# Optimization experiments

Hardware: AMD Instinct MI355X
Metric: run time of the kernel (lower is better)

The kernel has to match this reference:

```python
import jax, jax.numpy as jnp
import numpy as np

HIDDEN = 4096
NUM_HEADS = 32
NUM_KV_HEADS = 8
HEAD_DIM = 128
ROPE_THETA = 1000000.0
EPS = 1e-6


def setup_inputs() -> dict:
    key = jax.random.key(0)
    ks = jax.random.split(key, 6)
    B, S = 1, 2048
    s = 0.02
    return {
        "hidden_states": jax.random.normal(ks[0], (B, S, HIDDEN), dtype=jnp.float32),
        "position_ids": jnp.arange(B * S, dtype=jnp.int64).reshape(B, S),
        "Wq": jax.random.normal(ks[1], (HIDDEN, NUM_HEADS * HEAD_DIM), dtype=jnp.float32) * s,
        "Wk": jax.random.normal(ks[2], (HIDDEN, NUM_KV_HEADS * HEAD_DIM), dtype=jnp.float32) * s,
        "Wv": jax.random.normal(ks[3], (HIDDEN, NUM_KV_HEADS * HEAD_DIM), dtype=jnp.float32) * s,
        "Wo": jax.random.normal(ks[4], (NUM_HEADS * HEAD_DIM, HIDDEN), dtype=jnp.float32) * s,
        "q_norm_w": jnp.ones((HEAD_DIM,), dtype=jnp.float32),
        "k_norm_w": jnp.ones((HEAD_DIM,), dtype=jnp.float32),
    }


def _rmsnorm(x, w):
    var = jnp.mean(jnp.square(x.astype(jnp.float32)), axis=-1, keepdims=True)
    xn = x * jax.lax.rsqrt(var + EPS)
    return (w * xn).astype(x.dtype)


def _apply_rope(x, positions):
    # x: [b, h, s, d]; positions: [b, s]
    d = x.shape[-1]
    inv_freq = 1.0 / (ROPE_THETA ** (jnp.arange(0, d, 2, dtype=jnp.float32) / d))
    freqs = positions.astype(jnp.float32)[..., None] * inv_freq  # [b, s, d/2]
    cos = jnp.cos(freqs)[:, None].astype(x.dtype)  # [b, 1, s, d/2]
    sin = jnp.sin(freqs)[:, None].astype(x.dtype)
    x1, x2 = x[..., : d // 2], x[..., d // 2 :]
    return jnp.concatenate([x1 * cos - x2 * sin, x2 * cos + x1 * sin], axis=-1)


def reference(hidden_states, position_ids, Wq, Wk, Wv, Wo, q_norm_w, k_norm_w):
    B, S, _ = hidden_states.shape
    groups = NUM_HEADS // NUM_KV_HEADS

    q = (hidden_states @ Wq).reshape(B, S, NUM_HEADS, HEAD_DIM).transpose(0, 2, 1, 3)
    k = (hidden_states @ Wk).reshape(B, S, NUM_KV_HEADS, HEAD_DIM).transpose(0, 2, 1, 3)
    v = (hidden_states @ Wv).reshape(B, S, NUM_KV_HEADS, HEAD_DIM).transpose(0, 2, 1, 3)

    q = _rmsnorm(q, q_norm_w)
    k = _rmsnorm(k, k_norm_w)
    q = _apply_rope(q, position_ids)
    k = _apply_rope(k, position_ids)

    new_k, new_v = k, v  # returned cache (no past_key_value)

    # GQA expansion: [b, kvh, s, d] -> [b, h, s, d]
    kx = jnp.repeat(k, groups, axis=1)
    vx = jnp.repeat(v, groups, axis=1)

    scale = 1.0 / (HEAD_DIM ** 0.5)
    scores = jnp.einsum("bhqd,bhkd->bhqk", q, kx) * scale  # [b, h, s, s]

    kv_len = kx.shape[2]
    row = jnp.arange(S)[:, None]
    col = jnp.arange(kv_len)[None, :]
    causal = col <= row + (kv_len - S)
    scores = jnp.where(causal, scores, -jnp.inf)

    probs = jax.nn.softmax(scores.astype(jnp.float32), axis=-1).astype(q.dtype)
    attn = jnp.einsum("bhqk,bhkd->bhqd", probs, vx)  # [b, h, s, d]
    attn = attn.transpose(0, 2, 1, 3).reshape(B, S, NUM_HEADS * HEAD_DIM)
    out = attn @ Wo
    return out, new_k, new_v, probs
```

## Files before the change

### kernel.cpp

```cpp
#include <hip/hip_runtime.h>
#include <hip/hip_bf16.h>
#include <stdint.h>

#define S_LEN 2048
#define HID   4096
#define NH    32
#define NKV   8
#define HD    128
#define SCALE 0.08838834764831845f

using bf16   = __hip_bfloat16;
using bf16x8 = __attribute__((ext_vector_type(8))) __bf16;
using f32x4  = __attribute__((ext_vector_type(4))) float;

__device__ __forceinline__ void gl2lds(const void* g, void* l) {
  __builtin_amdgcn_global_load_lds(
      (const __attribute__((address_space(1))) unsigned int*)(uintptr_t)g,
      (__attribute__((address_space(3))) unsigned int*)(uintptr_t)l, 16, 0, 0);
}

__device__ __forceinline__ f32x4 mfma16(bf16x8 a, bf16x8 b, f32x4 c) {
  return __builtin_amdgcn_mfma_f32_16x16x32_bf16(a, b, c, 0, 0, 0);
}

__global__ void cast_f32_bf16(const float* __restrict__ in, bf16* __restrict__ out) {
  size_t i = ((size_t)blockIdx.x * 256 + threadIdx.x) * 4;
  float4 v = *(const float4*)(in + i);
  __hip_bfloat162 a, b;
  a.x = __float2bfloat16(v.x); a.y = __float2bfloat16(v.y);
  b.x = __float2bfloat16(v.z); b.y = __float2bfloat16(v.w);
  *(__hip_bfloat162*)(out + i)     = a;
  *(__hip_bfloat162*)(out + i + 2) = b;
}

__global__ void transpose_cast(const float* __restrict__ in, bf16* __restrict__ out,
                               int K, int N) {
  __shared__ float tile[64][65];
  int n0 = blockIdx.x * 64, k0 = blockIdx.y * 64;
  for (int i = 0; i < 16; i++) {
    int lin = i * 256 + threadIdx.x;
    int r = lin >> 6, c = lin & 63;
    tile[r][c] = in[(size_t)(k0 + r) * N + n0 + c];
  }
  __syncthreads();
  for (int i = 0; i < 16; i++) {
    int lin = i * 256 + threadIdx.x;
    int r = lin >> 6, c = lin & 63;
    out[(size_t)(n0 + r) * K + k0 + c] = __float2bfloat16(tile[c][r]);
  }
}

template <int EPI>
__global__ __launch_bounds__(256) void gemm_bt(const bf16* __restrict__ A,
                                               const bf16* __restrict__ Bt,
                                               float* __restrict__ C,
                                               bf16* __restrict__ Caux,
                                               int M, int N, int K) {
  __shared__ bf16 Asm[128 * 32];
  __shared__ bf16 Bsm[128 * 32];
  const int tid = threadIdx.x;
  const int lane = tid & 63, wv = tid >> 6;
  const int quad = lane >> 4, l16 = lane & 15;
  const int wm = wv >> 1, wn = wv & 1;
  const size_t bm = (size_t)blockIdx.y * 128, bn = (size_t)blockIdx.x * 128;
  const bf16* Ab = A + bm * K;
  const bf16* Bb = Bt + bn * K;
  f32x4 acc[4][4];
  for (int i = 0; i < 4; i++)
    for (int j = 0; j < 4; j++) acc[i][j] = 0.f;
  const int c0 = tid, c1 = 256 + tid;
  const int r0 = c0 >> 2, kc0 = (c0 & 3) << 3;
  const int r1 = c1 >> 2, kc1 = (c1 & 3) << 3;
  for (int k0 = 0; k0 < K; k0 += 32) {
    gl2lds(Ab + (size_t)r0 * K + k0 + kc0, (char*)Asm + c0 * 16);
    gl2lds(Ab + (size_t)r1 * K + k0 + kc1, (char*)Asm + c1 * 16);
    gl2lds(Bb + (size_t)r0 * K + k0 + kc0, (char*)Bsm + c0 * 16);
    gl2lds(Bb + (size_t)r1 * K + k0 + kc1, (char*)Bsm + c1 * 16);
    __syncthreads();
    bf16x8 af[4], bfr[4];
    for (int t = 0; t < 4; t++) {
      af[t]  = *(const bf16x8*)(Asm + (wm * 64 + t * 16 + l16) * 32 + quad * 8);
      bfr[t] = *(const bf16x8*)(Bsm + (wn * 64 + t * 16 + l16) * 32 + quad * 8);
    }
    for (int mt = 0; mt < 4; mt++)
      for (int nt = 0; nt < 4; nt++)
        acc[mt][nt] = mfma16(af[mt], bfr[nt], acc[mt][nt]);
    __syncthreads();
  }
  for (int mt = 0; mt < 4; mt++)
    for (int nt = 0; nt < 4; nt++)
      for (int r = 0; r < 4; r++) {
        size_t mm = bm + wm * 64 + mt * 16 + quad * 4 + r;
        size_t nn = bn + wn * 64 + nt * 16 + l16;
        float v = acc[mt][nt][r];
        if constexpr (EPI == 0) {
          C[mm * N + nn] = v;
        } else {
          int hh = (int)(nn >> 7), dd = (int)(nn & 127);
          C[((size_t)hh * S_LEN + mm) * HD + dd] = v;
          Caux[((size_t)hh * HD + dd) * S_LEN + mm] = __float2bfloat16(v);
        }
      }
}

__global__ __launch_bounds__(256) void norm_rope(const float* __restrict__ xin,
                                                 const float* __restrict__ w,
                                                 const int* __restrict__ pos,
                                                 bf16* __restrict__ xbf,
                                                 float* __restrict__ fout, int nh) {
  const int wv = threadIdx.x >> 6, lane = threadIdx.x & 63;
  const int row = blockIdx.x * 4 + wv;
  const int t = row / nh, h = row - t * nh;
  float2 x = *(const float2*)(xin + (size_t)row * 128 + lane * 2);
  float ss = x.x * x.x + x.y * x.y;
  for (int off = 32; off >= 1; off >>= 1) ss += __shfl_xor(ss, off, 64);
  float rr = rsqrtf(ss * (1.f / 128.f) + 1e-6f);
  float2 wv2 = *(const float2*)(w + lane * 2);
  float xn0 = x.x * rr * wv2.x, xn1 = x.y * rr * wv2.y;
  float p = (float)pos[t];
  int i0 = (lane & 31) * 2;
  const float k = 13.815510557964274f / 64.f;
  float f0 = p * expf(-(float)i0 * k);
  float f1 = p * expf(-(float)(i0 + 1) * k);
  float c0 = cosf(f0), s0 = sinf(f0), c1 = cosf(f1), s1 = sinf(f1);
  float y0 = __shfl_xor(xn0, 32, 64), y1 = __shfl_xor(xn1, 32, 64);
  float o0, o1;
  if (lane < 32) { o0 = xn0 * c0 - y0 * s0; o1 = xn1 * c1 - y1 * s1; }
  else           { o0 = xn0 * c0 + y0 * s0; o1 = xn1 * c1 + y1 * s1; }
  size_t ob = ((size_t)h * S_LEN + t) * 128 + lane * 2;
  __hip_bfloat162 bb;
  bb.x = __float2bfloat16(o0); bb.y = __float2bfloat16(o1);
  *(__hip_bfloat162*)(xbf + ob) = bb;
  if (fout) { float2 f2; f2.x = o0; f2.y = o1; *(float2*)(fout + ob) = f2; }
}

__global__ __launch_bounds__(256) void attn_kernel(const bf16* __restrict__ qb,
                                                   const bf16* __restrict__ kb,
                                                   const bf16* __restrict__ vt,
                                                   float* __restrict__ probs,
                                                   bf16* __restrict__ attnb) {
  __shared__ bf16 Ksm[64 * 128];
  __shared__ bf16 Vsm[128 * 64];
  __shared__ bf16 Psm[4 * 16 * 72];
  const int h = blockIdx.y, bq = blockIdx.x;
  const int hk = h >> 2;
  const int tid = threadIdx.x;
  const int lane = tid & 63, wv = tid >> 6;
  const int quad = lane >> 4, l16 = lane & 15;
  const int q0 = bq * 64, rbase = q0 + wv * 16;

  bf16x8 qf[4];
  {
    const bf16* qp = qb + ((size_t)h * S_LEN + rbase + l16) * HD + quad * 8;
    for (int ks = 0; ks < 4; ks++) qf[ks] = *(const bf16x8*)(qp + ks * 32);
  }
  const bf16* kbase = kb + (size_t)hk * S_LEN * HD;
  const bf16* vbase = vt + (size_t)hk * HD * S_LEN;

  float m[4], l[4];
  for (int r = 0; r < 4; r++) { m[r] = -1e30f; l[r] = 0.f; }

  for (int kt = 0; kt <= bq; kt++) {
    for (int i = 0; i < 4; i++) {
      int c = i * 256 + tid;
      int krow = c >> 4, j = c & 15;
      gl2lds(kbase + (size_t)kt * 8192 + (size_t)krow * 128 + ((j ^ (krow & 7)) << 3),
             (char*)Ksm + c * 16);
    }
    __syncthreads();
    f32x4 s[4];
    for (int nt = 0; nt < 4; nt++) s[nt] = 0.f;
    for (int ks = 0; ks < 4; ks++)
      for (int nt = 0; nt < 4; nt++) {
        int krow = nt * 16 + l16;
        int slot = (ks * 4 + quad) ^ (krow & 7);
        bf16x8 kf = *(const bf16x8*)(Ksm + krow * 128 + slot * 8);
        s[nt] = mfma16(qf[ks], kf, s[nt]);
      }
    for (int r = 0; r < 4; r++) {
      const int rowg = rbase + quad * 4 + r;
      float vv[4], tm = -1e30f;
      for (int nt = 0; nt < 4; nt++) {
        int col = kt * 64 + nt * 16 + l16;
        float v = s[nt][r] * SCALE;
        v = (col <= rowg) ? v : -1e30f;
        vv[nt] = v;
        tm = fmaxf(tm, v);
      }
      for (int off = 1; off < 16; off <<= 1) tm = fmaxf(tm, __shfl_xor(tm, off, 64));
      float nm = fmaxf(m[r], tm);
      float se = 0.f;
      for (int nt = 0; nt < 4; nt++) se += __expf(vv[nt] - nm);
      for (int off = 1; off < 16; off <<= 1) se += __shfl_xor(se, off, 64);
      l[r] = l[r] * __expf(m[r] - nm) + se;
      m[r] = nm;
    }
    __syncthreads();
  }

  float invl[4];
  for (int r = 0; r < 4; r++) invl[r] = 1.f / l[r];
  f32x4 o[8];
  for (int n2 = 0; n2 < 8; n2++) o[n2] = 0.f;

  for (int kt = 0; kt < 32; kt++) {
    if (kt > bq) {
      for (int r = 0; r < 4; r++) {
        float* pp = probs + ((size_t)h * S_LEN + rbase + quad * 4 + r) * S_LEN + kt * 64 + l16;
        for (int nt = 0; nt < 4; nt++) pp[nt * 16] = 0.f;
      }
      continue;
    }
    for (int i = 0; i < 4; i++) {
      int c = i * 256 + tid;
      int krow = c >> 4, j = c & 15;
      gl2lds(kbase + (size_t)kt * 8192 + (size_t)krow * 128 + ((j ^ (krow & 7)) << 3),
             (char*)Ksm + c * 16);
      int d = c >> 3, jv = c & 7;
      gl2lds(vbase + (size_t)d * S_LEN + kt * 64 + ((jv ^ (d & 7)) << 3),
             (char*)Vsm + c * 16);
    }
    __syncthreads();
    f32x4 s[4];
    for (int nt = 0; nt < 4; nt++) s[nt] = 0.f;
    for (int ks = 0; ks < 4; ks++)
      for (int nt = 0; nt < 4; nt++) {
        int krow = nt * 16 + l16;
        int slot = (ks * 4 + quad) ^ (krow & 7);
        bf16x8 kf = *(const bf16x8*)(Ksm + krow * 128 + slot * 8);
        s[nt] = mfma16(qf[ks], kf, s[nt]);
      }
    for (int r = 0; r < 4; r++) {
      const int rowg = rbase + quad * 4 + r;
      float* pp = probs + ((size_t)h * S_LEN + rowg) * S_LEN + kt * 64;
      for (int nt = 0; nt < 4; nt++) {
        int col = kt * 64 + nt * 16 + l16;
        float p = (col <= rowg) ? __expf(s[nt][r] * SCALE - m[r]) * invl[r] : 0.f;
        pp[nt * 16 + l16] = p;
        Psm[wv * 1152 + (quad * 4 + r) * 72 + nt * 16 + l16] = __float2bfloat16(p);
      }
    }
    asm volatile("s_waitcnt lgkmcnt(0)" ::: "memory");
    bf16x8 pf0 = *(const bf16x8*)(Psm + wv * 1152 + l16 * 72 + quad * 8);
    bf16x8 pf1 = *(const bf16x8*)(Psm + wv * 1152 + l16 * 72 + 32 + quad * 8);
    for (int n2 = 0; n2 < 8; n2++) {
      int vrow = n2 * 16 + l16;
      int s0 = quad ^ (vrow & 7), s1 = (4 + quad) ^ (vrow & 7);
      bf16x8 vb0 = *(const bf16x8*)(Vsm + vrow * 64 + s0 * 8);
      bf16x8 vb1 = *(const bf16x8*)(Vsm + vrow * 64 + s1 * 8);
      o[n2] = mfma16(pf0, vb0, o[n2]);
      o[n2] = mfma16(pf1, vb1, o[n2]);
    }
    __syncthreads();
  }
  for (int n2 = 0; n2 < 8; n2++)
    for (int r = 0; r < 4; r++)
      attnb[((size_t)(rbase + quad * 4 + r)) * HID + h * HD + n2 * 16 + l16] =
          __float2bfloat16(o[n2][r]);
}

extern "C" void kernel_launch(void* const* d_in, const int* in_sizes, int n_in,
                              void* d_out, int out_size, void* d_ws, size_t ws_size,
                              hipStream_t stream) {
  const float* hidden = (const float*)d_in[0];
  const int*   pos    = (const int*)d_in[1];
  const float* Wq     = (const float*)d_in[2];
  const float* Wk     = (const float*)d_in[3];
  const float* Wv     = (const float*)d_in[4];
  const float* Wo     = (const float*)d_in[5];
  const float* qw     = (const float*)d_in[6];
  const float* kw     = (const float*)d_in[7];

  float* out   = (float*)d_out;
  float* newk  = out + (size_t)S_LEN * HID;
  float* newv  = newk + (size_t)NKV * S_LEN * HD;
  float* probs = newv + (size_t)NKV * S_LEN * HD;

  char* w = (char*)d_ws;
  bf16* hb   = (bf16*)w;  w += (size_t)S_LEN * HID * 2;
  bf16* wqt  = (bf16*)w;  w += (size_t)HID * HID * 2;
  bf16* wkt  = (bf16*)w;  w += (size_t)1024 * HID * 2;
  bf16* wvt  = (bf16*)w;  w += (size_t)1024 * HID * 2;
  float* qraw = (float*)w; w += (size_t)S_LEN * HID * 4;
  float* kraw = (float*)w; w += (size_t)S_LEN * 1024 * 4;
  bf16* vtb  = (bf16*)w;  w += (size_t)NKV * HD * S_LEN * 2;
  bf16* qbf   = hb;
  bf16* wot   = wqt;
  bf16* kbf   = wkt;
  bf16* attnb = (bf16*)qraw;

  cast_f32_bf16<<<(S_LEN * HID) / 1024, 256, 0, stream>>>(hidden, hb);
  transpose_cast<<<dim3(HID / 64, HID / 64), 256, 0, stream>>>(Wq, wqt, HID, HID);
  transpose_cast<<<dim3(1024 / 64, HID / 64), 256, 0, stream>>>(Wk, wkt, HID, 1024);
  transpose_cast<<<dim3(1024 / 64, HID / 64), 256, 0, stream>>>(Wv, wvt, HID, 1024);

  gemm_bt<0><<<dim3(HID / 128, S_LEN / 128), 256, 0, stream>>>(hb, wqt, qraw, nullptr, S_LEN, HID, HID);
  gemm_bt<0><<<dim3(1024 / 128, S_LEN / 128), 256, 0, stream>>>(hb, wkt, kraw, nullptr, S_LEN, 1024, HID);
  gemm_bt<1><<<dim3(1024 / 128, S_LEN / 128), 256, 0, stream>>>(hb, wvt, newv, vtb, S_LEN, 1024, HID);

  norm_rope<<<(S_LEN * NKV) / 4, 256, 0, stream>>>(kraw, kw, pos, kbf, newk, NKV);
  norm_rope<<<(S_LEN * NH) / 4, 256, 0, stream>>>(qraw, qw, pos, qbf, nullptr, NH);
  transpose_cast<<<dim3(HID / 64, HID / 64), 256, 0, stream>>>(Wo, wot, HID, HID);

  attn_kernel<<<dim3(32, 32), 256, 0, stream>>>(qbf, kbf, vtb, probs, attnb);
  gemm_bt<0><<<dim3(HID / 128, S_LEN / 128), 256, 0, stream>>>(attnb, wot, out, nullptr, S_LEN, HID, HID);
}
```

Baseline: 1.330 ms.

## Fuse QKV GEMM, transpose attention MFMA layout, drop max pass, vectorize transpose

```diff
diff --git a/kernel.cpp b/kernel.cpp
--- a/kernel.cpp
+++ b/kernel.cpp
@@ -33,20 +33,26 @@
   *(__hip_bfloat162*)(out + i + 2) = b;
 }
 
-__global__ void transpose_cast(const float* __restrict__ in, bf16* __restrict__ out,
-                               int K, int N) {
-  __shared__ float tile[64][65];
-  int n0 = blockIdx.x * 64, k0 = blockIdx.y * 64;
-  for (int i = 0; i < 16; i++) {
-    int lin = i * 256 + threadIdx.x;
-    int r = lin >> 6, c = lin & 63;
-    tile[r][c] = in[(size_t)(k0 + r) * N + n0 + c];
+__global__ __launch_bounds__(256) void transpose_cast(const float* __restrict__ in,
+                                                      bf16* __restrict__ out,
+                                                      int K, int N) {
+  __shared__ float tile[64][69];
+  const int n0 = blockIdx.x * 64, k0 = blockIdx.y * 64;
+  const int rr = threadIdx.x >> 4, cc = (threadIdx.x & 15) * 4;
+  for (int i = 0; i < 4; i++) {
+    int r = i * 16 + rr;
+    float4 v = *(const float4*)(in + (size_t)(k0 + r) * N + n0 + cc);
+    tile[r][cc] = v.x; tile[r][cc + 1] = v.y; tile[r][cc + 2] = v.z; tile[r][cc + 3] = v.w;
   }
   __syncthreads();
-  for (int i = 0; i < 16; i++) {
-    int lin = i * 256 + threadIdx.x;
-    int r = lin >> 6, c = lin & 63;
-    out[(size_t)(n0 + r) * K + k0 + c] = __float2bfloat16(tile[c][r]);
+  for (int i = 0; i < 4; i++) {
+    int n = i * 16 + rr;
+    union { unsigned long long u8; unsigned short us[4]; } pk;
+    for (int j = 0; j < 4; j++) {
+      bf16 b = __float2bfloat16(tile[cc + j][n]);
+      pk.us[j] = *(unsigned short*)&b;
+    }
+    *(unsigned long long*)(out + (size_t)(n0 + n) * K + k0 + cc) = pk.u8;
   }
 }
 
@@ -54,6 +60,8 @@
 __global__ __launch_bounds__(256) void gemm_bt(const bf16* __restrict__ A,
                                                const bf16* __restrict__ Bt,
                                                float* __restrict__ C,
+                                               float* __restrict__ C2,
+                                               float* __restrict__ C3,
                                                bf16* __restrict__ Caux,
                                                int M, int N, int K) {
   __shared__ bf16 Asm[128 * 32];
@@ -96,9 +104,18 @@
         if constexpr (EPI == 0) {
           C[mm * N + nn] = v;
         } else {
-          int hh = (int)(nn >> 7), dd = (int)(nn & 127);
-          C[((size_t)hh * S_LEN + mm) * HD + dd] = v;
-          Caux[((size_t)hh * HD + dd) * S_LEN + mm] = __float2bfloat16(v);
+          if (bn < 4096) {
+            C[mm * 4096 + nn] = v;
+          } else if (bn < 5120) {
+            C2[mm * 1024 + (nn - 4096)] = v;
+          } else {
+            int nl = (int)(nn - 5120);
+            int hh = nl >> 7, dd = nl & 127;
+            C3[((size_t)hh * S_LEN + mm) * HD + dd] = v;
+            int t = (int)mm;
+            int tp = (t & ~31) + (((t & 15) >> 2) * 8) + (t & 3) + ((t & 16) >> 2);
+            Caux[((size_t)hh * HD + dd) * S_LEN + tp] = __float2bfloat16(v);
+          }
         }
       }
 }
@@ -141,25 +158,22 @@
                                                    bf16* __restrict__ attnb) {
   __shared__ bf16 Ksm[64 * 128];
   __shared__ bf16 Vsm[128 * 64];
-  __shared__ bf16 Psm[4 * 16 * 72];
-  const int h = blockIdx.y, bq = blockIdx.x;
+  const int h = blockIdx.y, bq = 31 - blockIdx.x;
   const int hk = h >> 2;
   const int tid = threadIdx.x;
   const int lane = tid & 63, wv = tid >> 6;
   const int quad = lane >> 4, l16 = lane & 15;
-  const int q0 = bq * 64, rbase = q0 + wv * 16;
+  const int g = bq * 64 + wv * 16 + l16;
 
   bf16x8 qf[4];
   {
-    const bf16* qp = qb + ((size_t)h * S_LEN + rbase + l16) * HD + quad * 8;
+    const bf16* qp = qb + ((size_t)h * S_LEN + g) * HD + quad * 8;
     for (int ks = 0; ks < 4; ks++) qf[ks] = *(const bf16x8*)(qp + ks * 32);
   }
   const bf16* kbase = kb + (size_t)hk * S_LEN * HD;
   const bf16* vbase = vt + (size_t)hk * HD * S_LEN;
 
-  float m[4], l[4];
-  for (int r = 0; r < 4; r++) { m[r] = -1e30f; l[r] = 0.f; }
-
+  float L = 0.f;
   for (int kt = 0; kt <= bq; kt++) {
     for (int i = 0; i < 4; i++) {
       int c = i * 256 + tid;
@@ -169,46 +183,33 @@
     }
     __syncthreads();
     f32x4 s[4];
-    for (int nt = 0; nt < 4; nt++) s[nt] = 0.f;
+    for (int mt = 0; mt < 4; mt++) s[mt] = 0.f;
     for (int ks = 0; ks < 4; ks++)
-      for (int nt = 0; nt < 4; nt++) {
-        int krow = nt * 16 + l16;
-        int slot = (ks * 4 + quad) ^ (krow & 7);
-        bf16x8 kf = *(const bf16x8*)(Ksm + krow * 128 + slot * 8);
-        s[nt] = mfma16(qf[ks], kf, s[nt]);
-      }
-    for (int r = 0; r < 4; r++) {
-      const int rowg = rbase + quad * 4 + r;
-      float vv[4], tm = -1e30f;
-      for (int nt = 0; nt < 4; nt++) {
-        int col = kt * 64 + nt * 16 + l16;
-        float v = s[nt][r] * SCALE;
-        v = (col <= rowg) ? v : -1e30f;
-        vv[nt] = v;
-        tm = fmaxf(tm, v);
-      }
-      for (int off = 1; off < 16; off <<= 1) tm = fmaxf(tm, __shfl_xor(tm, off, 64));
-      float nm = fmaxf(m[r], tm);
-      float se = 0.f;
-      for (int nt = 0; nt < 4; nt++) se += __expf(vv[nt] - nm);
-      for (int off = 1; off < 16; off <<= 1) se += __shfl_xor(se, off, 64);
-      l[r] = l[r] * __expf(m[r] - nm) + se;
-      m[r] = nm;
-    }
-    __syncthreads();
-  }
-
-  float invl[4];
-  for (int r = 0; r < 4; r++) invl[r] = 1.f / l[r];
+      for (int mt = 0; mt < 4; mt++) {
+        int tok = mt * 16 + l16;
+        int slot = (ks * 4 + quad) ^ (tok & 7);
+        bf16x8 kf = *(const bf16x8*)(Ksm + tok * 128 + slot * 8);
+        s[mt] = mfma16(kf, qf[ks], s[mt]);
+      }
+    for (int mt = 0; mt < 4; mt++)
+      for (int r = 0; r < 4; r++) {
+        int tk = kt * 64 + mt * 16 + quad * 4 + r;
+        if (tk <= g) L += __expf(s[mt][r] * SCALE);
+      }
+    __syncthreads();
+  }
+  L += __shfl_xor(L, 16, 64);
+  L += __shfl_xor(L, 32, 64);
+  const float invl = 1.f / L;
+
   f32x4 o[8];
-  for (int n2 = 0; n2 < 8; n2++) o[n2] = 0.f;
+  for (int dt = 0; dt < 8; dt++) o[dt] = 0.f;
 
   for (int kt = 0; kt < 32; kt++) {
+    float* pbase = probs + ((size_t)h * S_LEN + g) * S_LEN + kt * 64;
     if (kt > bq) {
-      for (int r = 0; r < 4; r++) {
-        float* pp = probs + ((size_t)h * S_LEN + rbase + quad * 4 + r) * S_LEN + kt * 64 + l16;
-        for (int nt = 0; nt < 4; nt++) pp[nt * 16] = 0.f;
-      }
+      f32x4 z = 0.f;
+      for (int mt = 0; mt < 4; mt++) *(f32x4*)(pbase + mt * 16 + quad * 4) = z;
       continue;
     }
     for (int i = 0; i < 4; i++) {
@@ -222,41 +223,45 @@
     }
     __syncthreads();
     f32x4 s[4];
-    for (int nt = 0; nt < 4; nt++) s[nt] = 0.f;
+    for (int mt = 0; mt < 4; mt++) s[mt] = 0.f;
     for (int ks = 0; ks < 4; ks++)
-      for (int nt = 0; nt < 4; nt++) {
-        int krow = nt * 16 + l16;
-        int slot = (ks * 4 + quad) ^ (krow & 7);
-        bf16x8 kf = *(const bf16x8*)(Ksm + krow * 128 + slot * 8);
-        s[nt] = mfma16(qf[ks], kf, s[nt]);
-      }
+      for (int mt = 0; mt < 4; mt++) {
+        int tok = mt * 16 + l16;
+        int slot = (ks * 4 + quad) ^ (tok & 7);
+        bf16x8 kf = *(const bf16x8*)(Ksm + tok * 128 + slot * 8);
+        s[mt] = mfma16(kf, qf[ks], s[mt]);
+      }
+    f32x4 p[4];
+    for (int mt = 0; mt < 4; mt++) {
+      for (int r = 0; r < 4; r++) {
+        int tk = kt * 64 + mt * 16 + quad * 4 + r;
+        p[mt][r] = (tk <= g) ? __expf(s[mt][r] * SCALE) * invl : 0.f;
+      }
+      *(f32x4*)(pbase + mt * 16 + quad * 4) = p[mt];
+    }
+    for (int kstep = 0; kstep < 2; kstep++) {
+      union { bf16x8 v; bf16 hh[8]; } pb;
+      for (int j = 0; j < 4; j++) {
+        pb.hh[j]     = __float2bfloat16(p[2 * kstep][j]);
+        pb.hh[4 + j] = __float2bfloat16(p[2 * kstep + 1][j]);
+      }
+      for (int dt = 0; dt < 8; dt++) {
+        int d = dt * 16 + l16;
+        int slot = (kstep * 4 + quad) ^ (d & 7);
+        bf16x8 vb = *(const bf16x8*)(Vsm + d * 64 + slot * 8);
+        o[dt] = mfma16(vb, pb.v, o[dt]);
+      }
+    }
+    __syncthreads();
+  }
+  for (int dt = 0; dt < 8; dt++) {
+    union { unsigned long long u8; unsigned short us[4]; } pk;
     for (int r = 0; r < 4; r++) {
-      const int rowg = rbase + quad * 4 + r;
-      float* pp = probs + ((size_t)h * S_LEN + rowg) * S_LEN + kt * 64;
-      for (int nt = 0; nt < 4; nt++) {
-        int col = kt * 64 + nt * 16 + l16;
-        float p = (col <= rowg) ? __expf(s[nt][r] * SCALE - m[r]) * invl[r] : 0.f;
-        pp[nt * 16 + l16] = p;
-        Psm[wv * 1152 + (quad * 4 + r) * 72 + nt * 16 + l16] = __float2bfloat16(p);
-      }
-    }
-    asm volatile("s_waitcnt lgkmcnt(0)" ::: "memory");
-    bf16x8 pf0 = *(const bf16x8*)(Psm + wv * 1152 + l16 * 72 + quad * 8);
-    bf16x8 pf1 = *(const bf16x8*)(Psm + wv * 1152 + l16 * 72 + 32 + quad * 8);
-    for (int n2 = 0; n2 < 8; n2++) {
-      int vrow = n2 * 16 + l16;
-      int s0 = quad ^ (vrow & 7), s1 = (4 + quad) ^ (vrow & 7);
-      bf16x8 vb0 = *(const bf16x8*)(Vsm + vrow * 64 + s0 * 8);
-      bf16x8 vb1 = *(const bf16x8*)(Vsm + vrow * 64 + s1 * 8);
-      o[n2] = mfma16(pf0, vb0, o[n2]);
-      o[n2] = mfma16(pf1, vb1, o[n2]);
-    }
-    __syncthreads();
-  }
-  for (int n2 = 0; n2 < 8; n2++)
-    for (int r = 0; r < 4; r++)
-      attnb[((size_t)(rbase + quad * 4 + r)) * HID + h * HD + n2 * 16 + l16] =
-          __float2bfloat16(o[n2][r]);
+      bf16 b = __float2bfloat16(o[dt][r]);
+      pk.us[r] = *(unsigned short*)&b;
+    }
+    *(unsigned long long*)(attnb + (size_t)g * HID + h * HD + dt * 16 + quad * 4) = pk.u8;
+  }
 }
 
 extern "C" void kernel_launch(void* const* d_in, const int* in_sizes, int n_in,
@@ -288,20 +293,21 @@
   bf16* wot   = wqt;
   bf16* kbf   = wkt;
   bf16* attnb = (bf16*)qraw;
+  bf16* wqkv  = wqt;
 
   cast_f32_bf16<<<(S_LEN * HID) / 1024, 256, 0, stream>>>(hidden, hb);
   transpose_cast<<<dim3(HID / 64, HID / 64), 256, 0, stream>>>(Wq, wqt, HID, HID);
   transpose_cast<<<dim3(1024 / 64, HID / 64), 256, 0, stream>>>(Wk, wkt, HID, 1024);
   transpose_cast<<<dim3(1024 / 64, HID / 64), 256, 0, stream>>>(Wv, wvt, HID, 1024);
 
-  gemm_bt<0><<<dim3(HID / 128, S_LEN / 128), 256, 0, stream>>>(hb, wqt, qraw, nullptr, S_LEN, HID, HID);
-  gemm_bt<0><<<dim3(1024 / 128, S_LEN / 128), 256, 0, stream>>>(hb, wkt, kraw, nullptr, S_LEN, 1024, HID);
-  gemm_bt<1><<<dim3(1024 / 128, S_LEN / 128), 256, 0, stream>>>(hb, wvt, newv, vtb, S_LEN, 1024, HID);
+  gemm_bt<2><<<dim3(6144 / 128, S_LEN / 128), 256, 0, stream>>>(
+      hb, wqkv, qraw, kraw, newv, vtb, S_LEN, 6144, HID);
 
   norm_rope<<<(S_LEN * NKV) / 4, 256, 0, stream>>>(kraw, kw, pos, kbf, newk, NKV);
   norm_rope<<<(S_LEN * NH) / 4, 256, 0, stream>>>(qraw, qw, pos, qbf, nullptr, NH);
   transpose_cast<<<dim3(HID / 64, HID / 64), 256, 0, stream>>>(Wo, wot, HID, HID);
 
   attn_kernel<<<dim3(32, 32), 256, 0, stream>>>(qbf, kbf, vtb, probs, attnb);
-  gemm_bt<0><<<dim3(HID / 128, S_LEN / 128), 256, 0, stream>>>(attnb, wot, out, nullptr, S_LEN, HID, HID);
-}
+  gemm_bt<0><<<dim3(HID / 128, S_LEN / 128), 256, 0, stream>>>(
+      attnb, wot, out, nullptr, nullptr, nullptr, S_LEN, HID, HID);
+}
```

After: 1.179 ms. 1.13x faster.
